# Performance work log

Hardware: AMD Instinct MI355X
Metric: run time of the kernel (lower is better)

## Reference

```python
import jax, jax.numpy as jnp
import numpy as np

LRELU = 0.2
EPS_LN = 1e-5
EPS_BN = 1e-5


def _seg_softmax(logits, seg, n):
    # softmax over edges grouped by destination node (PyG softmax), logits [E,H]
    m = jax.ops.segment_max(logits, seg, num_segments=n)
    e = jnp.exp(logits - m[seg])
    s = jax.ops.segment_sum(e, seg, num_segments=n)
    return e / (s[seg] + 1e-16)


def _gat(x, src, dst, n, W, a_src, a_dst, b, H, C):
    # PyG GATConv, concat=False (mean over heads), leaky_relu slope 0.2
    h = (x @ W).reshape(n, H, C)
    e = (h * a_src).sum(-1)[src] + (h * a_dst).sum(-1)[dst]  # [E,H]
    e = jnp.where(e > 0, e, LRELU * e)
    alpha = _seg_softmax(e, dst, n)
    out = jax.ops.segment_sum(h[src] * alpha[:, :, None], dst, num_segments=n)  # [N,H,C]
    return out.mean(1) + b


def _gcn(x, src, dst, n, W, b):
    # PyG GCNConv with symmetric normalization; edge list already contains self loops
    deg = jax.ops.segment_sum(jnp.ones(src.shape, x.dtype), dst, num_segments=n)
    dis = jnp.where(deg > 0, jax.lax.rsqrt(jnp.maximum(deg, 1e-12)), 0.0)
    h = x @ W
    w = (dis[src] * dis[dst])[:, None]
    return jax.ops.segment_sum(h[src] * w, dst, num_segments=n) + b


def _ln(x, g, b):
    mu = x.mean(-1, keepdims=True)
    v = x.var(-1, keepdims=True)
    return (x - mu) * jax.lax.rsqrt(v + EPS_LN) * g + b


def _bn_eval(x, g, b, rm, rv):
    return (x - rm) * jax.lax.rsqrt(rv + EPS_BN) * g + b


def _forward(x, edge_index, gin, bti, rmi, rvi, W1, as1, ad1, b1, Wg1, bg1,
             W2, as2, ad2, b2, Wg2, bg2, Ws, bs, Wf, bf,
             g1, be1, g2, be2, g3, be3, Wc1, bc1, gbn, bbn, rmb, rvb, Wc2, bc2):
    n = x.shape[0]
    xn = _bn_eval(x, gin, bti, rmi, rvi)
    sl = jnp.arange(n, dtype=edge_index.dtype)
    src = jnp.concatenate([edge_index[0], sl])
    dst = jnp.concatenate([edge_index[1], sl])
    # GAT1 (4 heads, 128) -> LN -> relu
    x1 = _gat(xn, src, dst, n, W1, as1, ad1, b1, 4, 128)
    x1 = jax.nn.relu(_ln(x1, g1, be1))
    # GCN1 -> relu
    x1g = jax.nn.relu(_gcn(x1, src, dst, n, Wg1, bg1))
    # GAT2 (2 heads, 64) -> LN -> relu
    x2 = _gat(x1g, src, dst, n, W2, as2, ad2, b2, 2, 64)
    x2 = jax.nn.relu(_ln(x2, g2, be2))
    # GCN2 -> relu
    x2g = jax.nn.relu(_gcn(x2, src, dst, n, Wg2, bg2))
    # skip + fusion
    skip = jax.nn.relu(xn @ Ws + bs)
    fused = jax.nn.relu(jnp.concatenate([x1g, x2g], axis=1) @ Wf + bf)
    final = _ln(fused + skip, g3, be3)
    # classifier: Linear -> BN(eval) -> relu -> Linear
    h = jax.nn.relu(_bn_eval(final @ Wc1 + bc1, gbn, bbn, rmb, rvb))
    return h @ Wc2 + bc2


def setup_inputs():
    key = jax.random.key(0)
    ks = jax.random.split(key, 20)
    N, F, E = 20000, 512, 160000
    H1, C1, H2, C2 = 4, 128, 2, 64
    rn = lambda k, sh, s=0.05: (jax.random.normal(k, sh) * s).astype(jnp.float32)
    return dict(
        x=jax.random.normal(ks[0], (N, F), jnp.float32),
        edge_index=jax.random.randint(ks[1], (2, E), 0, N, jnp.int32),
        gin=jnp.ones((F,), jnp.float32), bti=jnp.zeros((F,), jnp.float32),
        rmi=rn(ks[2], (F,)), rvi=(jax.random.uniform(ks[3], (F,)) + 0.5).astype(jnp.float32),
        W1=rn(ks[4], (F, H1 * C1)), as1=rn(ks[5], (H1, C1)), ad1=rn(ks[6], (H1, C1)), b1=jnp.zeros((C1,), jnp.float32),
        Wg1=rn(ks[7], (C1, C1)), bg1=jnp.zeros((C1,), jnp.float32),
        W2=rn(ks[8], (C1, H2 * C2)), as2=rn(ks[9], (H2, C2)), ad2=rn(ks[10], (H2, C2)), b2=jnp.zeros((C2,), jnp.float32),
        Wg2=rn(ks[11], (C2, C2)), bg2=jnp.zeros((C2,), jnp.float32),
        Ws=rn(ks[12], (F, C2)), bs=jnp.zeros((C2,), jnp.float32),
        Wf=rn(ks[13], (C1 + C2, C2)), bf=jnp.zeros((C2,), jnp.float32),
        g1=jnp.ones((C1,), jnp.float32), be1=jnp.zeros((C1,), jnp.float32),
        g2=jnp.ones((C2,), jnp.float32), be2=jnp.zeros((C2,), jnp.float32),
        g3=jnp.ones((C2,), jnp.float32), be3=jnp.zeros((C2,), jnp.float32),
        Wc1=rn(ks[14], (C2, 32)), bc1=jnp.zeros((32,), jnp.float32),
        gbn=jnp.ones((32,), jnp.float32), bbn=jnp.zeros((32,), jnp.float32),
        rmb=rn(ks[15], (32,)), rvb=(jax.random.uniform(ks[16], (32,)) + 0.5).astype(jnp.float32),
        Wc2=rn(ks[17], (32, 5)), bc2=jnp.zeros((5,), jnp.float32),
    )


def reference(x, edge_index, gin, bti, rmi, rvi, W1, as1, ad1, b1, Wg1, bg1,
              W2, as2, ad2, b2, Wg2, bg2, Ws, bs, Wf, bf,
              g1, be1, g2, be2, g3, be3, Wc1, bc1, gbn, bbn, rmb, rvb, Wc2, bc2):
    return _forward(x, edge_index, gin, bti, rmi, rvi, W1, as1, ad1, b1, Wg1, bg1,
                    W2, as2, ad2, b2, Wg2, bg2, Ws, bs, Wf, bf,
                    g1, be1, g2, be2, g3, be3, Wc1, bc1, gbn, bbn, rmb, rvb, Wc2, bc2)
```

## Files before the change

### kernel.cpp

```cpp
#include <hip/hip_runtime.h>
#include <hip/hip_bf16.h>

#define N_NODES 20000
#define F_IN 512

typedef __attribute__((ext_vector_type(8))) short short8;
typedef __attribute__((ext_vector_type(4))) float f32x4;

__device__ __forceinline__ ushort f2bf(float f) {
    uint u = __float_as_uint(f);
    u += 0x7FFF + ((u >> 16) & 1);
    return (ushort)(u >> 16);
}
__device__ __forceinline__ float bf2f(ushort h) { return __uint_as_float((uint)h << 16); }

__device__ __forceinline__ void gload_lds16(const void* g, void* l) {
    __builtin_amdgcn_global_load_lds(
        (const __attribute__((address_space(1))) void*)g,
        (__attribute__((address_space(3))) void*)l, 16, 0, 0);
}

__global__ void zero_int_k(int* p, int n) {
    int i = blockIdx.x * blockDim.x + threadIdx.x;
    if (i < n) p[i] = 0;
}

__global__ void hist_k(const int* __restrict__ ei, int E0, int N, int* __restrict__ deg) {
    int e = blockIdx.x * blockDim.x + threadIdx.x;
    int Etot = E0 + N;
    if (e >= Etot) return;
    int dst = (e < E0) ? ei[E0 + e] : (e - E0);
    atomicAdd(&deg[dst], 1);
}

__global__ __launch_bounds__(1024) void scan_k(const int* __restrict__ deg, int* __restrict__ rp,
                                               int* __restrict__ fp, float* __restrict__ dis,
                                               int N, int Etot) {
    __shared__ int part[1024];
    int tid = threadIdx.x;
    int chunk = (N + 1023) / 1024;
    int lo = tid * chunk, hi = min(lo + chunk, N);
    int s = 0;
    for (int i = lo; i < hi; i++) s += deg[i];
    part[tid] = s;
    __syncthreads();
    for (int off = 1; off < 1024; off <<= 1) {
        int t = 0;
        if (tid >= off) t = part[tid - off];
        __syncthreads();
        part[tid] += t;
        __syncthreads();
    }
    int run = part[tid] - s;
    for (int i = lo; i < hi; i++) {
        rp[i] = run; fp[i] = run;
        int d = deg[i];
        dis[i] = (d > 0) ? rsqrtf((float)d) : 0.f;
        run += d;
    }
    if (tid == 1023) { rp[N] = Etot; fp[N] = Etot; }
}

__global__ void scatter_k(const int* __restrict__ ei, int E0, int N, int* __restrict__ fp,
                          int* __restrict__ csr_src) {
    int e = blockIdx.x * blockDim.x + threadIdx.x;
    int Etot = E0 + N;
    if (e >= Etot) return;
    int src, dst;
    if (e < E0) { src = ei[e]; dst = ei[E0 + e]; }
    else        { src = e - E0; dst = src; }
    int pos = atomicAdd(&fp[dst], 1);
    csr_src[pos] = src;
}

__global__ void bnprep_k(const float* __restrict__ g, const float* __restrict__ b,
                         const float* __restrict__ rm, const float* __restrict__ rv,
                         float* __restrict__ sc, float* __restrict__ sh, int n) {
    int i = blockIdx.x * blockDim.x + threadIdx.x;
    if (i >= n) return;
    float s = g[i] * rsqrtf(rv[i] + 1e-5f);
    sc[i] = s;
    sh[i] = b[i] - rm[i] * s;
}

__global__ void splitA_k(const float* __restrict__ x, const float* __restrict__ sc,
                         const float* __restrict__ sh, ushort* __restrict__ Ah,
                         ushort* __restrict__ Al, int M, int Mpad) {
    size_t i4 = (size_t)blockIdx.x * blockDim.x + threadIdx.x;
    size_t base = i4 * 4;
    if (base >= (size_t)Mpad * 512) return;
    int row = (int)(base >> 9);
    ushort4 ah = {0, 0, 0, 0}, al = {0, 0, 0, 0};
    if (row < M) {
        float4 v = *(const float4*)&x[base];
        int c = (int)(base & 511);
        float f0 = v.x * sc[c] + sh[c];
        float f1 = v.y * sc[c + 1] + sh[c + 1];
        float f2 = v.z * sc[c + 2] + sh[c + 2];
        float f3 = v.w * sc[c + 3] + sh[c + 3];
        ah.x = f2bf(f0); al.x = f2bf(f0 - bf2f(ah.x));
        ah.y = f2bf(f1); al.y = f2bf(f1 - bf2f(ah.y));
        ah.z = f2bf(f2); al.z = f2bf(f2 - bf2f(ah.z));
        ah.w = f2bf(f3); al.w = f2bf(f3 - bf2f(ah.w));
    }
    *(ushort4*)&Ah[base] = ah;
    *(ushort4*)&Al[base] = al;
}

__global__ __launch_bounds__(256) void splitBt_k(const float* __restrict__ W1, const float* __restrict__ Ws,
                                                 ushort* __restrict__ Bth, ushort* __restrict__ Btl) {
    __shared__ float tile[64][65];
    int n0 = blockIdx.x * 64;
    int k0 = blockIdx.y * 64;
    int t = threadIdx.x;
    int a = t >> 6, b = t & 63;
#pragma unroll
    for (int i = 0; i < 16; i++) {
        int kk = a + i * 4, nn = b;
        int gk = k0 + kk, gn = n0 + nn;
        float v;
        if (gn < 512)      v = W1[(size_t)gk * 512 + gn];
        else if (gn < 576) v = Ws[(size_t)gk * 64 + (gn - 512)];
        else               v = 0.f;
        tile[kk][nn] = v;
    }
    __syncthreads();
#pragma unroll
    for (int i = 0; i < 16; i++) {
        int nn = a + i * 4, kk = b;
        float v = tile[kk][nn];
        ushort hi = f2bf(v);
        ushort lo = f2bf(v - bf2f(hi));
        Bth[(size_t)(n0 + nn) * 512 + k0 + kk] = hi;
        Btl[(size_t)(n0 + nn) * 512 + k0 + kk] = lo;
    }
}

__global__ __launch_bounds__(256) void mfma_gemm_k(
    const ushort* __restrict__ Ah, const ushort* __restrict__ Al,
    const ushort* __restrict__ Bth, const ushort* __restrict__ Btl,
    const float* __restrict__ bs, float* __restrict__ h1, float* __restrict__ skip,
    int M, int K) {
    __shared__ ushort Ah_s[128 * 32];
    __shared__ ushort Al_s[128 * 32];
    __shared__ ushort Bh_s[128 * 32];
    __shared__ ushort Bl_s[128 * 32];
    int t = threadIdx.x;
    int w = t >> 6, l = t & 63;

    int nwg = gridDim.x;
    int q = nwg >> 3, r = nwg & 7;
    int xcd = blockIdx.x & 7, lid = blockIdx.x >> 3;
    int wg = (xcd < r) ? xcd * (q + 1) + lid : r * (q + 1) + (xcd - r) * q + lid;
    int by = wg / 5, bx = wg % 5;
    int bm = by * 128;
    int n0 = bx * 128;
    int r0 = (w & 1) * 64, c0 = (w >> 1) * 64;

    f32x4 acc[4][4] = {};

    int kg_t = t >> 7;
    int row_t = t & 127;
    const size_t ga1 = (size_t)(bm + row_t) * 512 + kg_t * 8;
    const size_t ga2 = (size_t)(bm + row_t) * 512 + (kg_t + 2) * 8;
    const size_t gb1 = (size_t)(n0 + row_t) * 512 + kg_t * 8;
    const size_t gb2 = (size_t)(n0 + row_t) * 512 + (kg_t + 2) * 8;
    int elem0 = t * 8;

    for (int kt = 0; kt < K; kt += 32) {
        gload_lds16(Ah + ga1 + kt, &Ah_s[elem0]);
        gload_lds16(Ah + ga2 + kt, &Ah_s[elem0 + 2048]);
        gload_lds16(Al + ga1 + kt, &Al_s[elem0]);
        gload_lds16(Al + ga2 + kt, &Al_s[elem0 + 2048]);
        gload_lds16(Bth + gb1 + kt, &Bh_s[elem0]);
        gload_lds16(Bth + gb2 + kt, &Bh_s[elem0 + 2048]);
        gload_lds16(Btl + gb1 + kt, &Bl_s[elem0]);
        gload_lds16(Btl + gb2 + kt, &Bl_s[elem0 + 2048]);
        __syncthreads();

        short8 ah[4], al4[4], bh[4], bl[4];
        int kgl = l >> 4;
        int lr = l & 15;
#pragma unroll
        for (int f = 0; f < 4; f++) {
            int ra = kgl * 1024 + (r0 + f * 16 + lr) * 8;
            ah[f]  = *(const short8*)&Ah_s[ra];
            al4[f] = *(const short8*)&Al_s[ra];
            int rb = kgl * 1024 + (c0 + f * 16 + lr) * 8;
            bh[f] = *(const short8*)&Bh_s[rb];
            bl[f] = *(const short8*)&Bl_s[rb];
        }
#pragma unroll
        for (int fm = 0; fm < 4; fm++)
#pragma unroll
            for (int fn = 0; fn < 4; fn++) {
                acc[fm][fn] = __builtin_amdgcn_mfma_f32_16x16x32_bf16(ah[fm], bh[fn], acc[fm][fn], 0, 0, 0);
                acc[fm][fn] = __builtin_amdgcn_mfma_f32_16x16x32_bf16(ah[fm], bl[fn], acc[fm][fn], 0, 0, 0);
                acc[fm][fn] = __builtin_amdgcn_mfma_f32_16x16x32_bf16(al4[fm], bh[fn], acc[fm][fn], 0, 0, 0);
            }
        __syncthreads();
    }

#pragma unroll
    for (int fm = 0; fm < 4; fm++) {
        int row_base = bm + r0 + fm * 16 + (l >> 4) * 4;
#pragma unroll
        for (int fn = 0; fn < 4; fn++) {
            int col = n0 + c0 + fn * 16 + (l & 15);
#pragma unroll
            for (int r2 = 0; r2 < 4; r2++) {
                int row = row_base + r2;
                if (row < M) {
                    float v = acc[fm][fn][r2];
                    if (col < 512) h1[(size_t)row * 512 + col] = v;
                    else if (col < 576) skip[(size_t)row * 64 + (col - 512)] = fmaxf(v + bs[col - 512], 0.f);
                }
            }
        }
    }
}

template <int K, int NOUT>
__global__ __launch_bounds__(NOUT) void rowgemm_k(const float* __restrict__ X, const float* __restrict__ W,
                                                  float* __restrict__ out, int N) {
    __shared__ float Ws[K * NOUT];
    __shared__ float Xs[8][K];
    int c = threadIdx.x;
    for (int i = c; i < K * NOUT; i += NOUT) Ws[i] = W[i];
    for (int r0 = blockIdx.x * 8; r0 < N; r0 += gridDim.x * 8) {
        int nr = min(8, N - r0);
        __syncthreads();
        for (int i = c; i < nr * K; i += NOUT) Xs[i / K][i % K] = X[(size_t)r0 * K + i];
        __syncthreads();
        float acc[8] = {};
        for (int k = 0; k < K; k++) {
            float w = Ws[k * NOUT + c];
#pragma unroll
            for (int r = 0; r < 8; r++) acc[r] += Xs[r][k] * w;
        }
        for (int r = 0; r < nr; r++) out[(size_t)(r0 + r) * NOUT + c] = acc[r];
    }
}

template <int H, int C>
__global__ __launch_bounds__(256) void scores_k(const float* __restrict__ h, const float* __restrict__ a_src,
                                                const float* __restrict__ a_dst, float* __restrict__ ss,
                                                float* __restrict__ sd, int N) {
    int wid = (blockIdx.x * blockDim.x + threadIdx.x) >> 6;
    int lane = threadIdx.x & 63;
    if (wid >= N * H) return;
    int hh = wid % H;
    const float* hp = h + (size_t)(wid / H) * (H * C) + hh * C;
    float s1 = 0.f, s2 = 0.f;
    for (int c = lane; c < C; c += 64) {
        float v = hp[c];
        s1 += v * a_src[hh * C + c];
        s2 += v * a_dst[hh * C + c];
    }
#pragma unroll
    for (int off = 32; off; off >>= 1) {
        s1 += __shfl_down(s1, off);
        s2 += __shfl_down(s2, off);
    }
    if (lane == 0) { ss[wid] = s1; sd[wid] = s2; }
}

template <int H, int C>
__global__ __launch_bounds__(C) void gat_agg_k(const float* __restrict__ h, const float* __restrict__ ss,
                                               const float* __restrict__ sd, const float* __restrict__ bias,
                                               const float* __restrict__ g, const float* __restrict__ be,
                                               const int* __restrict__ rp, const int* __restrict__ csr_src,
                                               float* __restrict__ out, int N) {
    int n = blockIdx.x;
    int tid = threadIdx.x;
    __shared__ float m_s[H], s_s[H], red[4];
    __shared__ int srcs[64];
    __shared__ float aw[64 * H];
    int e0 = rp[n], deg = rp[n + 1] - e0;
    bool small = (deg <= 64);
    int hh = tid >> 5, l = tid & 31;

    if (small && tid < deg) srcs[tid] = csr_src[e0 + tid];
    __syncthreads();

    float sdv = sd[n * H + hh];
    float m = -1e30f, s = 0.f;
    for (int k = l; k < deg; k += 32) {
        int src = small ? srcs[k] : csr_src[e0 + k];
        float e = ss[src * H + hh] + sdv;
        e = (e > 0.f) ? e : 0.2f * e;
        if (small) aw[k * H + hh] = e;
        float mn = fmaxf(m, e);
        s = s * __expf(m - mn) + __expf(e - mn);
        m = mn;
    }
#pragma unroll
    for (int off = 16; off; off >>= 1) {
        float mo = __shfl_xor(m, off), so = __shfl_xor(s, off);
        float mn = fmaxf(m, mo);
        s = s * __expf(m - mn) + so * __expf(mo - mn);
        m = mn;
    }
    if (l == 0) { m_s[hh] = m; s_s[hh] = s + 1e-16f; }
    __syncthreads();

    float v = 0.f;
    if (small) {
        for (int idx = tid; idx < deg * H; idx += C) {
            int h2 = idx & (H - 1);
            aw[idx] = __expf(aw[idx] - m_s[h2]) / s_s[h2];
        }
        __syncthreads();
        for (int k = 0; k < deg; k++) {
            const float* hp = h + (size_t)srcs[k] * (H * C) + tid;
#pragma unroll
            for (int h2 = 0; h2 < H; h2++) v += aw[k * H + h2] * hp[h2 * C];
        }
    } else {
        for (int t0 = 0; t0 < deg; t0 += 64) {
            int tl = min(64, deg - t0);
            __syncthreads();
            if (tid < tl) srcs[tid] = csr_src[e0 + t0 + tid];
            __syncthreads();
            for (int idx = tid; idx < tl * H; idx += C) {
                int k = idx / H, h2 = idx & (H - 1);
                float e = ss[srcs[k] * H + h2] + sd[n * H + h2];
                e = (e > 0.f) ? e : 0.2f * e;
                aw[idx] = __expf(e - m_s[h2]) / s_s[h2];
            }
            __syncthreads();
            for (int k = 0; k < tl; k++) {
                const float* hp = h + (size_t)srcs[k] * (H * C) + tid;
#pragma unroll
                for (int h2 = 0; h2 < H; h2++) v += aw[k * H + h2] * hp[h2 * C];
            }
        }
    }

    v = v * (1.f / H) + bias[tid];
    float t1 = v;
#pragma unroll
    for (int off = 32; off; off >>= 1) t1 += __shfl_xor(t1, off);
    float mu;
    if (C == 128) {
        if ((tid & 63) == 0) red[tid >> 6] = t1;
        __syncthreads();
        mu = (red[0] + red[1]) * (1.f / C);
    } else {
        mu = t1 * (1.f / C);
    }
    float d = v - mu;
    float t2 = d * d;
#pragma unroll
    for (int off = 32; off; off >>= 1) t2 += __shfl_xor(t2, off);
    float var;
    if (C == 128) {
        if ((tid & 63) == 0) red[2 + (tid >> 6)] = t2;
        __syncthreads();
        var = (red[2] + red[3]) * (1.f / C);
    } else {
        var = t2 * (1.f / C);
    }
    float y = d * rsqrtf(var + 1e-5f) * g[tid] + be[tid];
    out[(size_t)n * C + tid] = fmaxf(y, 0.f);
}

template <int C>
__global__ __launch_bounds__(C) void gcn_agg_k(const float* __restrict__ h, const float* __restrict__ dis,
                                               const float* __restrict__ bias, const int* __restrict__ rp,
                                               const int* __restrict__ csr_src, float* __restrict__ out, int N) {
    int n = blockIdx.x;
    int tid = threadIdx.x;
    __shared__ int srcs[64];
    __shared__ float w[64];
    int e0 = rp[n], deg = rp[n + 1] - e0;
    float dn = dis[n];
    float acc = 0.f;
    for (int t0 = 0; t0 < deg; t0 += 64) {
        int tl = min(64, deg - t0);
        if (tid < tl) {
            int s = csr_src[e0 + t0 + tid];
            srcs[tid] = s;
            w[tid] = dis[s] * dn;
        }
        __syncthreads();
        for (int k = 0; k < tl; k++) acc += w[k] * h[(size_t)srcs[k] * C + tid];
        __syncthreads();
    }
    out[(size_t)n * C + tid] = fmaxf(acc + bias[tid], 0.f);
}

__global__ __launch_bounds__(64) void final_fused_k(
    const float* __restrict__ hg2, const float* __restrict__ dis, const float* __restrict__ bg2,
    const int* __restrict__ rp, const int* __restrict__ csr_src,
    const float* __restrict__ x1g, const float* __restrict__ Wf, const float* __restrict__ bf,
    const float* __restrict__ skip, const float* __restrict__ g3, const float* __restrict__ be3,
    const float* __restrict__ Wc1, const float* __restrict__ bc1, const float* __restrict__ gbn,
    const float* __restrict__ bbn, const float* __restrict__ rmb, const float* __restrict__ rvb,
    const float* __restrict__ Wc2, const float* __restrict__ bc2, float* __restrict__ out, int N) {
    int n = blockIdx.x;
    int tid = threadIdx.x;
    __shared__ int srcs[64];
    __shared__ float w[64];
    __shared__ float cat[192];
    __shared__ float fbuf[64];
    __shared__ float hbuf[32];
    int e0 = rp[n], deg = rp[n + 1] - e0;
    float dn = dis[n];
    float acc = 0.f;
    for (int t0 = 0; t0 < deg; t0 += 64) {
        int tl = min(64, deg - t0);
        if (tid < tl) {
            int s = csr_src[e0 + t0 + tid];
            srcs[tid] = s;
            w[tid] = dis[s] * dn;
        }
        __syncthreads();
        for (int k = 0; k < tl; k++) acc += w[k] * hg2[(size_t)srcs[k] * 64 + tid];
        __syncthreads();
    }
    float x2gv = fmaxf(acc + bg2[tid], 0.f);
    cat[tid] = x1g[(size_t)n * 128 + tid];
    cat[64 + tid] = x1g[(size_t)n * 128 + 64 + tid];
    cat[128 + tid] = x2gv;
    __syncthreads();
    float fa = bf[tid];
    for (int j = 0; j < 192; j++) fa += cat[j] * Wf[j * 64 + tid];
    fa = fmaxf(fa, 0.f) + skip[(size_t)n * 64 + tid];
    float t1 = fa;
#pragma unroll
    for (int off = 32; off; off >>= 1) t1 += __shfl_xor(t1, off);
    float mu = t1 * (1.f / 64.f);
    float d = fa - mu;
    float t2 = d * d;
#pragma unroll
    for (int off = 32; off; off >>= 1) t2 += __shfl_xor(t2, off);
    float var = t2 * (1.f / 64.f);
    fbuf[tid] = d * rsqrtf(var + 1e-5f) * g3[tid] + be3[tid];
    __syncthreads();
    if (tid < 32) {
        float a = bc1[tid];
        for (int j = 0; j < 64; j++) a += fbuf[j] * Wc1[j * 32 + tid];
        a = (a - rmb[tid]) * rsqrtf(rvb[tid] + 1e-5f) * gbn[tid] + bbn[tid];
        hbuf[tid] = fmaxf(a, 0.f);
    }
    __syncthreads();
    if (tid < 5) {
        float a = bc2[tid];
        for (int j = 0; j < 32; j++) a += hbuf[j] * Wc2[j * 5 + tid];
        out[(size_t)n * 5 + tid] = a;
    }
}

extern "C" void kernel_launch(void* const* d_in, const int* in_sizes, int n_in,
                              void* d_out, int out_size, void* d_ws, size_t ws_size,
                              hipStream_t stream) {
    const float* x   = (const float*)d_in[0];
    const int*   ei  = (const int*)d_in[1];
    const float* gin = (const float*)d_in[2];
    const float* bti = (const float*)d_in[3];
    const float* rmi = (const float*)d_in[4];
    const float* rvi = (const float*)d_in[5];
    const float* W1  = (const float*)d_in[6];
    const float* as1 = (const float*)d_in[7];
    const float* ad1 = (const float*)d_in[8];
    const float* b1  = (const float*)d_in[9];
    const float* Wg1 = (const float*)d_in[10];
    const float* bg1 = (const float*)d_in[11];
    const float* W2  = (const float*)d_in[12];
    const float* as2 = (const float*)d_in[13];
    const float* ad2 = (const float*)d_in[14];
    const float* b2  = (const float*)d_in[15];
    const float* Wg2 = (const float*)d_in[16];
    const float* bg2 = (const float*)d_in[17];
    const float* Ws  = (const float*)d_in[18];
    const float* bs  = (const float*)d_in[19];
    const float* Wf  = (const float*)d_in[20];
    const float* bf  = (const float*)d_in[21];
    const float* g1  = (const float*)d_in[22];
    const float* be1 = (const float*)d_in[23];
    const float* g2  = (const float*)d_in[24];
    const float* be2 = (const float*)d_in[25];
    const float* g3  = (const float*)d_in[26];
    const float* be3 = (const float*)d_in[27];
    const float* Wc1 = (const float*)d_in[28];
    const float* bc1 = (const float*)d_in[29];
    const float* gbn = (const float*)d_in[30];
    const float* bbn = (const float*)d_in[31];
    const float* rmb = (const float*)d_in[32];
    const float* rvb = (const float*)d_in[33];
    const float* Wc2 = (const float*)d_in[34];
    const float* bc2 = (const float*)d_in[35];
    float* out = (float*)d_out;

    const int N = in_sizes[0] / F_IN;
    const int E0 = in_sizes[1] / 2;
    const int Etot = E0 + N;
    const int Mpad = 20096;

    char* wp = (char*)d_ws;
    auto alloc = [&](size_t bytes) -> void* {
        void* p = (void*)wp;
        wp += (bytes + 255) & ~(size_t)255;
        return p;
    };
    float* h1   = (float*)alloc((size_t)N * 512 * 4);
    ushort* Ah  = (ushort*)alloc((size_t)Mpad * 512 * 2);
    ushort* Al  = (ushort*)alloc((size_t)Mpad * 512 * 2);
    ushort* Bth = (ushort*)alloc((size_t)640 * 512 * 2);
    ushort* Btl = (ushort*)alloc((size_t)640 * 512 * 2);
    float* skip = (float*)alloc((size_t)N * 64 * 4);
    float* ss1  = (float*)alloc((size_t)N * 4 * 4);
    float* sd1  = (float*)alloc((size_t)N * 4 * 4);
    float* ss2  = (float*)alloc((size_t)N * 2 * 4);
    float* sd2  = (float*)alloc((size_t)N * 2 * 4);
    float* dis  = (float*)alloc((size_t)N * 4);
    float* sc   = (float*)alloc((size_t)F_IN * 4);
    float* sh   = (float*)alloc((size_t)F_IN * 4);
    int* deg    = (int*)alloc((size_t)N * 4);
    int* rp     = (int*)alloc((size_t)(N + 1) * 4);
    int* fp     = (int*)alloc((size_t)(N + 1) * 4);
    int* csr    = (int*)alloc((size_t)Etot * 4);
    float* hg1 = h1;
    float* x1g = h1 + (size_t)N * 128;
    float* h2  = h1 + (size_t)N * 256;
    float* x2  = h1 + (size_t)N * 384;
    float* hg2 = h1 + (size_t)N * 448;
    float* x1  = (float*)Ah;

    zero_int_k<<<(N + 255) / 256, 256, 0, stream>>>(deg, N);
    hist_k<<<(Etot + 255) / 256, 256, 0, stream>>>(ei, E0, N, deg);
    scan_k<<<1, 1024, 0, stream>>>(deg, rp, fp, dis, N, Etot);
    scatter_k<<<(Etot + 255) / 256, 256, 0, stream>>>(ei, E0, N, fp, csr);
    bnprep_k<<<2, 256, 0, stream>>>(gin, bti, rmi, rvi, sc, sh, F_IN);
    splitA_k<<<(int)(((size_t)Mpad * 512 / 4 + 255) / 256), 256, 0, stream>>>(x, sc, sh, Ah, Al, N, Mpad);
    splitBt_k<<<dim3(10, 8), 256, 0, stream>>>(W1, Ws, Bth, Btl);

    mfma_gemm_k<<<785, 256, 0, stream>>>(Ah, Al, Bth, Btl, bs, h1, skip, N, 512);

    scores_k<4, 128><<<(N * 4 + 3) / 4, 256, 0, stream>>>(h1, as1, ad1, ss1, sd1, N);
    gat_agg_k<4, 128><<<N, 128, 0, stream>>>(h1, ss1, sd1, b1, g1, be1, rp, csr, x1, N);

    rowgemm_k<128, 128><<<1280, 128, 0, stream>>>(x1, Wg1, hg1, N);
    gcn_agg_k<128><<<N, 128, 0, stream>>>(hg1, dis, bg1, rp, csr, x1g, N);

    rowgemm_k<128, 128><<<1280, 128, 0, stream>>>(x1g, W2, h2, N);
    scores_k<2, 64><<<(N * 2 + 3) / 4, 256, 0, stream>>>(h2, as2, ad2, ss2, sd2, N);
    gat_agg_k<2, 64><<<N, 64, 0, stream>>>(h2, ss2, sd2, b2, g2, be2, rp, csr, x2, N);

    rowgemm_k<64, 64><<<1280, 64, 0, stream>>>(x2, Wg2, hg2, N);

    final_fused_k<<<N, 64, 0, stream>>>(hg2, dis, bg2, rp, csr, x1g, Wf, bf, skip, g3, be3,
                                        Wc1, bc1, gbn, bbn, rmb, rvb, Wc2, bc2, out, N);
}
```

Measured before the change: 577.1 us.

## Fuse GAT1 attention scores into MFMA GEMM epilogue and swizzle LDS layout

The first-layer GEMM now computes per-head source and destination attention scores in its epilogue, using warp shuffles and LDS atomics. This removes the separate scores kernel and its re-read of h1. The LDS staging is also reorganised into one merged hi/lo buffer per operand with an XOR swizzle, meant to reduce bank conflicts on the fragment reads. The cost is extra epilogue work, an added sync, and more index arithmetic in the load path.

Result: faster. 540.5 us (-6.3%).

```diff
diff --git a/kernel.cpp b/kernel.cpp
--- a/kernel.cpp
+++ b/kernel.cpp
@@ -139,12 +139,13 @@
 __global__ __launch_bounds__(256) void mfma_gemm_k(
     const ushort* __restrict__ Ah, const ushort* __restrict__ Al,
     const ushort* __restrict__ Bth, const ushort* __restrict__ Btl,
-    const float* __restrict__ bs, float* __restrict__ h1, float* __restrict__ skip,
+    const float* __restrict__ bs, const float* __restrict__ as1, const float* __restrict__ ad1,
+    float* __restrict__ h1, float* __restrict__ skip,
+    float* __restrict__ ss1, float* __restrict__ sd1,
     int M, int K) {
-    __shared__ ushort Ah_s[128 * 32];
-    __shared__ ushort Al_s[128 * 32];
-    __shared__ ushort Bh_s[128 * 32];
-    __shared__ ushort Bl_s[128 * 32];
+    __shared__ ushort A_s[128 * 64];
+    __shared__ ushort B_s[128 * 64];
+    __shared__ float s1buf[128], s2buf[128];
     int t = threadIdx.x;
     int w = t >> 6, l = t & 63;
 
@@ -159,36 +160,37 @@
 
     f32x4 acc[4][4] = {};
 
-    int kg_t = t >> 7;
-    int row_t = t & 127;
-    const size_t ga1 = (size_t)(bm + row_t) * 512 + kg_t * 8;
-    const size_t ga2 = (size_t)(bm + row_t) * 512 + (kg_t + 2) * 8;
-    const size_t gb1 = (size_t)(n0 + row_t) * 512 + kg_t * 8;
-    const size_t gb2 = (size_t)(n0 + row_t) * 512 + (kg_t + 2) * 8;
-    int elem0 = t * 8;
+    int sl = (t & 7) ^ ((t >> 3) & 7);
+    const ushort* aArr = (sl < 4) ? Ah : Al;
+    const ushort* bArr = (sl < 4) ? Bth : Btl;
+    int ko = (sl & 3) * 8;
+    size_t asrc[4], bsrc[4];
+#pragma unroll
+    for (int c = 0; c < 4; c++) {
+        int rr = c * 32 + (t >> 3);
+        asrc[c] = (size_t)(bm + rr) * 512 + ko;
+        bsrc[c] = (size_t)(n0 + rr) * 512 + ko;
+    }
+    int d0 = t * 8;
 
     for (int kt = 0; kt < K; kt += 32) {
-        gload_lds16(Ah + ga1 + kt, &Ah_s[elem0]);
-        gload_lds16(Ah + ga2 + kt, &Ah_s[elem0 + 2048]);
-        gload_lds16(Al + ga1 + kt, &Al_s[elem0]);
-        gload_lds16(Al + ga2 + kt, &Al_s[elem0 + 2048]);
-        gload_lds16(Bth + gb1 + kt, &Bh_s[elem0]);
-        gload_lds16(Bth + gb2 + kt, &Bh_s[elem0 + 2048]);
-        gload_lds16(Btl + gb1 + kt, &Bl_s[elem0]);
-        gload_lds16(Btl + gb2 + kt, &Bl_s[elem0 + 2048]);
+#pragma unroll
+        for (int c = 0; c < 4; c++) gload_lds16(aArr + asrc[c] + kt, &A_s[c * 2048 + d0]);
+#pragma unroll
+        for (int c = 0; c < 4; c++) gload_lds16(bArr + bsrc[c] + kt, &B_s[c * 2048 + d0]);
         __syncthreads();
 
         short8 ah[4], al4[4], bh[4], bl[4];
-        int kgl = l >> 4;
-        int lr = l & 15;
+        int lr = l & 15, kg = l >> 4;
+        int spa = kg ^ (lr & 7);
 #pragma unroll
         for (int f = 0; f < 4; f++) {
-            int ra = kgl * 1024 + (r0 + f * 16 + lr) * 8;
-            ah[f]  = *(const short8*)&Ah_s[ra];
-            al4[f] = *(const short8*)&Al_s[ra];
-            int rb = kgl * 1024 + (c0 + f * 16 + lr) * 8;
-            bh[f] = *(const short8*)&Bh_s[rb];
-            bl[f] = *(const short8*)&Bl_s[rb];
+            int ra = (r0 + f * 16 + lr) * 64;
+            ah[f]  = *(const short8*)&A_s[ra + spa * 8];
+            al4[f] = *(const short8*)&A_s[ra + (spa ^ 4) * 8];
+            int rb = (c0 + f * 16 + lr) * 64;
+            bh[f] = *(const short8*)&B_s[rb + spa * 8];
+            bl[f] = *(const short8*)&B_s[rb + (spa ^ 4) * 8];
         }
 #pragma unroll
         for (int fm = 0; fm < 4; fm++)
@@ -201,12 +203,13 @@
         __syncthreads();
     }
 
+    int lr = l & 15, kg = l >> 4;
 #pragma unroll
     for (int fm = 0; fm < 4; fm++) {
-        int row_base = bm + r0 + fm * 16 + (l >> 4) * 4;
+        int row_base = bm + r0 + fm * 16 + kg * 4;
 #pragma unroll
         for (int fn = 0; fn < 4; fn++) {
-            int col = n0 + c0 + fn * 16 + (l & 15);
+            int col = n0 + c0 + fn * 16 + lr;
 #pragma unroll
             for (int r2 = 0; r2 < 4; r2++) {
                 int row = row_base + r2;
@@ -217,6 +220,42 @@
                 }
             }
         }
+    }
+
+    if (t < 128) { s1buf[t] = 0.f; s2buf[t] = 0.f; }
+    __syncthreads();
+    if (bx < 4) {
+        float aw_[4], dw_[4];
+#pragma unroll
+        for (int fn = 0; fn < 4; fn++) {
+            int col = n0 + c0 + fn * 16 + lr;
+            aw_[fn] = as1[col];
+            dw_[fn] = ad1[col];
+        }
+#pragma unroll
+        for (int fm = 0; fm < 4; fm++)
+#pragma unroll
+            for (int r2 = 0; r2 < 4; r2++) {
+                float p1 = acc[fm][0][r2] * aw_[0] + acc[fm][1][r2] * aw_[1] +
+                           acc[fm][2][r2] * aw_[2] + acc[fm][3][r2] * aw_[3];
+                float p2 = acc[fm][0][r2] * dw_[0] + acc[fm][1][r2] * dw_[1] +
+                           acc[fm][2][r2] * dw_[2] + acc[fm][3][r2] * dw_[3];
+#pragma unroll
+                for (int off = 1; off < 16; off <<= 1) {
+                    p1 += __shfl_xor(p1, off);
+                    p2 += __shfl_xor(p2, off);
+                }
+                if (lr == 0) {
+                    int rloc = r0 + fm * 16 + kg * 4 + r2;
+                    atomicAdd(&s1buf[rloc], p1);
+                    atomicAdd(&s2buf[rloc], p2);
+                }
+            }
+    }
+    __syncthreads();
+    if (bx < 4 && t < 128 && bm + t < M) {
+        ss1[(size_t)(bm + t) * 4 + bx] = s1buf[t];
+        sd1[(size_t)(bm + t) * 4 + bx] = s2buf[t];
     }
 }
 
@@ -536,9 +575,8 @@
     splitA_k<<<(int)(((size_t)Mpad * 512 / 4 + 255) / 256), 256, 0, stream>>>(x, sc, sh, Ah, Al, N, Mpad);
     splitBt_k<<<dim3(10, 8), 256, 0, stream>>>(W1, Ws, Bth, Btl);
 
-    mfma_gemm_k<<<785, 256, 0, stream>>>(Ah, Al, Bth, Btl, bs, h1, skip, N, 512);
-
-    scores_k<4, 128><<<(N * 4 + 3) / 4, 256, 0, stream>>>(h1, as1, ad1, ss1, sd1, N);
+    mfma_gemm_k<<<785, 256, 0, stream>>>(Ah, Al, Bth, Btl, bs, as1, ad1, h1, skip, ss1, sd1, N, 512);
+
     gat_agg_k<4, 128><<<N, 128, 0, stream>>>(h1, ss1, sd1, b1, g1, be1, rp, csr, x1, N);
 
     rowgemm_k<128, 128><<<1280, 128, 0, stream>>>(x1, Wg1, hg1, N);
```
